# Optimization experiments

Hardware: AMD Instinct MI355X
Metric: run time of the kernel (lower is better)

Reference implementation:

```python
import jax, jax.numpy as jnp
import numpy as np

S = 512      # num_seg (queries)
T = 16384    # frames
D = 512      # d_model
DFF = 2048   # dim_feedforward
EPS = 1e-5


def layer_norm(x, g, b):
    mu = jnp.mean(x, axis=-1, keepdims=True)
    var = jnp.mean((x - mu) ** 2, axis=-1, keepdims=True)
    return (x - mu) * jax.lax.rsqrt(var + EPS) * g + b


def setup_inputs() -> dict:
    key = jax.random.key(0)
    ks = jax.random.split(key, 16)
    inv = 1.0 / np.sqrt(D)
    invf = 1.0 / np.sqrt(DFF)
    # action_idx: exactly S contiguous segments over T frames
    action_idx = (jnp.arange(T, dtype=jnp.int32) * S) // T
    return {
        "tgt": jax.random.normal(ks[0], (S, 1, D), jnp.float32),
        "memory": jax.random.normal(ks[1], (T, 1, D), jnp.float32),
        "pos": jax.random.normal(ks[2], (T, 1, D), jnp.float32),
        "query_pos": jax.random.normal(ks[3], (S, 1, D), jnp.float32),
        "action_idx": action_idx,
        "W_tgt2": jax.random.uniform(ks[4], (D, D), jnp.float32, -inv, inv),
        "b_tgt2": jax.random.uniform(ks[5], (D,), jnp.float32, -inv, inv),
        "W1": jax.random.uniform(ks[6], (DFF, D), jnp.float32, -inv, inv),
        "b1": jax.random.uniform(ks[7], (DFF,), jnp.float32, -inv, inv),
        "W2": jax.random.uniform(ks[8], (D, DFF), jnp.float32, -invf, invf),
        "b2": jax.random.uniform(ks[9], (D,), jnp.float32, -invf, invf),
        "g2": jnp.ones((D,), jnp.float32),
        "be2": jnp.zeros((D,), jnp.float32),
        "g3": jnp.ones((D,), jnp.float32),
        "be3": jnp.zeros((D,), jnp.float32),
    }


def reference(tgt, memory, pos, query_pos, action_idx,
              W_tgt2, b_tgt2, W1, b1, W2, b2, g2, be2, g3, be3):
    num_seg, _, dim = tgt.shape
    q = tgt + query_pos          # [S, 1, D]
    k = memory + pos             # [T, 1, D]
    v = memory                   # [T, 1, D]

    # segment-neighbor mask: seg_id per frame; query s attends to frames in
    # segments {s-1, s, s+1}
    change = jnp.concatenate([jnp.zeros((1,), jnp.int32),
                              (action_idx[1:] != action_idx[:-1]).astype(jnp.int32)])
    seg_id = jnp.cumsum(change)                                   # [T]
    mask = jnp.abs(seg_id[None, :] - jnp.arange(num_seg)[:, None]) <= 1  # [S, T]

    scores = jnp.einsum("sbd,tbd->bst", q, k) / np.sqrt(dim)      # [1, S, T]
    scores = jnp.where(mask[None], scores, -jnp.inf)
    attn = jax.nn.softmax(scores, axis=-1)                        # [1, S, T]

    ctx = jnp.einsum("bst,tbd->sbd", attn, v)                     # [S, 1, D]
    tgt2 = jax.nn.relu(ctx) @ W_tgt2.T + b_tgt2                   # [S, 1, D]
    x = layer_norm(tgt + tgt2, g2, be2)
    ffn = jax.nn.relu(x @ W1.T + b1) @ W2.T + b2
    out = layer_norm(x + ffn, g3, be3)
    return out
```

## Files before the change

### kernel.cpp

```cpp
#include <hip/hip_runtime.h>
#include <math.h>

#define S_Q  512
#define T_F  16384
#define D_M  512
#define DFF_ 2048
#define SEG  32
#define HSEG 16
#define SCALE 0.04419417382415922f

typedef __attribute__((ext_vector_type(8))) short short8;
typedef __attribute__((ext_vector_type(4))) float floatx4;

__device__ __forceinline__ unsigned short f2bf(float f) {
    unsigned int u = __builtin_bit_cast(unsigned int, f);
    u += 0x7FFFu + ((u >> 16) & 1u);
    return (unsigned short)(u >> 16);
}

__device__ __forceinline__ void async_copy16(const void* g, void* l) {
    __builtin_amdgcn_global_load_lds(
        (const __attribute__((address_space(1))) void*)g,
        (__attribute__((address_space(3))) void*)l, 16, 0, 0);
}

struct GSm { short A[2][2048]; short B[2][2048]; };

struct Params {
    const float *tgt, *memory, *pos, *qp;
    const float *b_tgt2, *b1, *b2, *g2, *be2, *g3, *be3;
    const float *W_tgt2, *W1, *W2;
    float *out;
    float *part; float2 *me;
    unsigned short *rc;
    float *gpart1, *x;
    unsigned short *xb, *h;
    float *gpart3;
    unsigned short *Wt2b, *W1b, *W2b;
};

__global__ __launch_bounds__(256, 4) void attn_conv(Params p)
{
    const int jb   = blockIdx.x;
    const int s    = jb >> 1;
    const int hh   = jb & 1;
    const int tid  = threadIdx.x;
    const int lane = tid & 63;
    const int wave = tid >> 6;

    __shared__ float v[HSEG * D_M];
    __shared__ float sc[3][HSEG];
    __shared__ float pr[3][HSEG];

    {
        const float* g = p.memory + (size_t)jb * HSEG * D_M
                       + (size_t)wave * 2048 + lane * 4;
        #pragma unroll
        for (int r = 0; r < 8; ++r)
            async_copy16(g + r * 256, v + wave * 2048 + r * 256);
    }

    float q0[8] = {}, q1[8] = {}, q2[8] = {};
    {
        const int d = lane * 8;
        if (s > 0) {
            const float4 a0 = *(const float4*)(p.tgt + (size_t)(s - 1) * D_M + d);
            const float4 a1 = *(const float4*)(p.tgt + (size_t)(s - 1) * D_M + d + 4);
            const float4 b0 = *(const float4*)(p.qp  + (size_t)(s - 1) * D_M + d);
            const float4 b1 = *(const float4*)(p.qp  + (size_t)(s - 1) * D_M + d + 4);
            q0[0]=a0.x+b0.x; q0[1]=a0.y+b0.y; q0[2]=a0.z+b0.z; q0[3]=a0.w+b0.w;
            q0[4]=a1.x+b1.x; q0[5]=a1.y+b1.y; q0[6]=a1.z+b1.z; q0[7]=a1.w+b1.w;
        }
        {
            const float4 a0 = *(const float4*)(p.tgt + (size_t)s * D_M + d);
            const float4 a1 = *(const float4*)(p.tgt + (size_t)s * D_M + d + 4);
            const float4 b0 = *(const float4*)(p.qp  + (size_t)s * D_M + d);
            const float4 b1 = *(const float4*)(p.qp  + (size_t)s * D_M + d + 4);
            q1[0]=a0.x+b0.x; q1[1]=a0.y+b0.y; q1[2]=a0.z+b0.z; q1[3]=a0.w+b0.w;
            q1[4]=a1.x+b1.x; q1[5]=a1.y+b1.y; q1[6]=a1.z+b1.z; q1[7]=a1.w+b1.w;
        }
        if (s < S_Q - 1) {
            const float4 a0 = *(const float4*)(p.tgt + (size_t)(s + 1) * D_M + d);
            const float4 a1 = *(const float4*)(p.tgt + (size_t)(s + 1) * D_M + d + 4);
            const float4 b0 = *(const float4*)(p.qp  + (size_t)(s + 1) * D_M + d);
            const float4 b1 = *(const float4*)(p.qp  + (size_t)(s + 1) * D_M + d + 4);
            q2[0]=a0.x+b0.x; q2[1]=a0.y+b0.y; q2[2]=a0.z+b0.z; q2[3]=a0.w+b0.w;
            q2[4]=a1.x+b1.x; q2[5]=a1.y+b1.y; q2[6]=a1.z+b1.z; q2[7]=a1.w+b1.w;
        }
    }
    __syncthreads();

    #pragma unroll
    for (int r = 0; r < 4; ++r) {
        const int f = wave * 4 + r;
        const size_t t = (size_t)(jb * HSEG + f);
        const float4 pA = *(const float4*)(p.pos + t * D_M + lane * 8);
        const float4 pB = *(const float4*)(p.pos + t * D_M + lane * 8 + 4);
        const float4 mA = *(const float4*)(v + f * D_M + lane * 8);
        const float4 mB = *(const float4*)(v + f * D_M + lane * 8 + 4);
        const float k8[8] = {mA.x+pA.x, mA.y+pA.y, mA.z+pA.z, mA.w+pA.w,
                             mB.x+pB.x, mB.y+pB.y, mB.z+pB.z, mB.w+pB.w};
        float a0 = 0.f, a1 = 0.f, a2 = 0.f;
        #pragma unroll
        for (int i = 0; i < 8; ++i) {
            a0 += k8[i] * q0[i]; a1 += k8[i] * q1[i]; a2 += k8[i] * q2[i];
        }
        #pragma unroll
        for (int off = 32; off > 0; off >>= 1) {
            a0 += __shfl_xor(a0, off, 64);
            a1 += __shfl_xor(a1, off, 64);
            a2 += __shfl_xor(a2, off, 64);
        }
        if (lane == 0) { sc[0][f] = a0 * SCALE; sc[1][f] = a1 * SCALE; sc[2][f] = a2 * SCALE; }
    }
    __syncthreads();

    if (wave < 3) {
        float mx = -1e30f;
        #pragma unroll
        for (int f = 0; f < HSEG; ++f) mx = fmaxf(mx, sc[wave][f]);
        float e = 0.f;
        #pragma unroll
        for (int f = 0; f < HSEG; ++f) {
            const float pe = __expf(sc[wave][f] - mx);
            e += pe;
            if (lane == 0) pr[wave][f] = pe;
        }
        const int q = s - 1 + wave;
        const int slot = hh + 4 - 2 * wave;
        if (lane == 0 && q >= 0 && q < S_Q)
            p.me[q * 6 + slot] = make_float2(mx, e);
    }
    __syncthreads();

    const int d0 = tid * 2;
    float c0x=0,c0y=0,c1x=0,c1y=0,c2x=0,c2y=0;
    #pragma unroll
    for (int f = 0; f < HSEG; ++f) {
        const float2 vv = *(const float2*)(v + f * D_M + d0);
        const float w0 = pr[0][f], w1 = pr[1][f], w2 = pr[2][f];
        c0x += w0 * vv.x; c0y += w0 * vv.y;
        c1x += w1 * vv.x; c1y += w1 * vv.y;
        c2x += w2 * vv.x; c2y += w2 * vv.y;
    }
    if (s > 0)
        *(float2*)(p.part + ((size_t)(s - 1) * 6 + 4 + hh) * D_M + d0) = make_float2(c0x, c0y);
    *(float2*)(p.part + ((size_t)s * 6 + 2 + hh) * D_M + d0) = make_float2(c1x, c1y);
    if (s < S_Q - 1)
        *(float2*)(p.part + ((size_t)(s + 1) * 6 + hh) * D_M + d0) = make_float2(c2x, c2y);

    {
        constexpr int n0 = D_M * D_M, n1 = DFF_ * D_M;
        constexpr int tot4 = (D_M * D_M + DFF_ * D_M + D_M * DFF_) / 4;
        for (int i4 = blockIdx.x * 256 + tid; i4 < tot4; i4 += 1024 * 256) {
            int i = i4 * 4;
            const float* src; unsigned short* dst;
            if (i < n0)            { src = p.W_tgt2; dst = p.Wt2b; }
            else if (i < n0 + n1)  { src = p.W1;     dst = p.W1b;  i -= n0; }
            else                   { src = p.W2;     dst = p.W2b;  i -= n0 + n1; }
            const float4 vv = *(const float4*)(src + i);
            unsigned short o[4] = {f2bf(vv.x), f2bf(vv.y), f2bf(vv.z), f2bf(vv.w)};
            *(uint2*)(dst + i) = *(const uint2*)o;
        }
    }
}

__global__ __launch_bounds__(256) void g_merge(Params p)
{
    const int row = blockIdx.x;
    const int tid = threadIdx.x;
    const int slo = (row == 0)       ? 2 : 0;
    const int shi = (row == S_Q - 1) ? 3 : 5;
    float mx = -1e30f;
    for (int s = slo; s <= shi; ++s) mx = fmaxf(mx, p.me[row * 6 + s].x);
    float den = 0.f, c[6] = {};
    for (int s = slo; s <= shi; ++s) {
        c[s] = __expf(p.me[row * 6 + s].x - mx);
        den += p.me[row * 6 + s].y * c[s];
    }
    const float inv = 1.f / den;
    const int d0 = tid * 2;
    float ax = 0.f, ay = 0.f;
    for (int s = slo; s <= shi; ++s) {
        const float2 pp = *(const float2*)(p.part + ((size_t)row * 6 + s) * D_M + d0);
        ax += c[s] * pp.x; ay += c[s] * pp.y;
    }
    const unsigned short o0 = f2bf(fmaxf(ax * inv, 0.f));
    const unsigned short o1 = f2bf(fmaxf(ay * inv, 0.f));
    *(unsigned int*)(p.rc + (size_t)row * D_M + d0) =
        (unsigned int)o0 | ((unsigned int)o1 << 16);
}

template<bool PARTIAL>
__device__ __forceinline__ void gemm_tile32(
    GSm* sg, const unsigned short* __restrict__ A, const unsigned short* __restrict__ B,
    int Nout, int K, int m0, int n0, int kbase, int niter,
    const float* __restrict__ bias, void* __restrict__ Cout, int zoff)
{
    const int tid  = threadIdx.x;
    const int lane = tid & 63;
    const int wave = tid >> 6;
    const int srow = tid >> 3;
    const int scol = (tid & 7) * 8;
    const int quad = lane >> 4;
    const int r16  = lane & 15;
    const int wm = (wave >> 1) * 16;
    const int wn = (wave & 1) * 16;

    floatx4 acc = {0.f, 0.f, 0.f, 0.f};

    async_copy16(A + (size_t)(m0 + srow) * K + kbase + scol, &sg->A[0][wave * 512]);
    async_copy16(B + (size_t)(n0 + srow) * K + kbase + scol, &sg->B[0][wave * 512]);

    for (int it = 0; it < niter; ++it) {
        __syncthreads();
        if (it + 1 < niter) {
            const int k0 = kbase + (it + 1) * 64;
            const int nb = (it + 1) & 1;
            async_copy16(A + (size_t)(m0 + srow) * K + k0 + scol, &sg->A[nb][wave * 512]);
            async_copy16(B + (size_t)(n0 + srow) * K + k0 + scol, &sg->B[nb][wave * 512]);
        }
        const short* Ab = sg->A[it & 1];
        const short* Bb = sg->B[it & 1];
        #pragma unroll
        for (int ks = 0; ks < 2; ++ks) {
            const short8 a = *(const short8*)(Ab + (wm + r16) * 64 + ks * 32 + quad * 8);
            const short8 b = *(const short8*)(Bb + (wn + r16) * 64 + ks * 32 + quad * 8);
            acc = __builtin_amdgcn_mfma_f32_16x16x32_bf16(a, b, acc, 0, 0, 0);
        }
    }

    const int col = n0 + wn + r16;
    const float bs = PARTIAL ? 0.f : bias[col];
    #pragma unroll
    for (int r = 0; r < 4; ++r) {
        const int row = m0 + wm + quad * 4 + r;
        float cv = acc[r];
        if (PARTIAL) {
            ((float*)Cout)[((size_t)(zoff + row)) * Nout + col] = cv;
        } else {
            cv = fmaxf(cv + bs, 0.f);
            ((unsigned short*)Cout)[(size_t)row * Nout + col] = f2bf(cv);
        }
    }
}

template<int NP, bool WRITE_BF16>
__device__ __forceinline__ void ln_rows(
    const float* __restrict__ parts, const float* __restrict__ res,
    const float* __restrict__ bias, const float* __restrict__ g,
    const float* __restrict__ be, float* __restrict__ out,
    unsigned short* __restrict__ out_bf, int rowblk)
{
    const int row  = rowblk * 4 + (threadIdx.x >> 6);
    const int lane = threadIdx.x & 63;

    float vv[8];
    #pragma unroll
    for (int hh = 0; hh < 2; ++hh) {
        const int d = lane * 8 + hh * 4;
        float4 a = *(const float4*)(res + (size_t)row * D_M + d);
        const float4 b = *(const float4*)(bias + d);
        a.x += b.x; a.y += b.y; a.z += b.z; a.w += b.w;
        #pragma unroll
        for (int z = 0; z < NP; ++z) {
            const float4 pp = *(const float4*)(parts + ((size_t)z * S_Q + row) * D_M + d);
            a.x += pp.x; a.y += pp.y; a.z += pp.z; a.w += pp.w;
        }
        vv[hh * 4 + 0] = a.x; vv[hh * 4 + 1] = a.y;
        vv[hh * 4 + 2] = a.z; vv[hh * 4 + 3] = a.w;
    }

    float sum = 0.f;
    #pragma unroll
    for (int i = 0; i < 8; ++i) sum += vv[i];
    #pragma unroll
    for (int off = 32; off > 0; off >>= 1) sum += __shfl_xor(sum, off, 64);
    const float mu = sum * (1.0f / 512.0f);

    float var = 0.f;
    #pragma unroll
    for (int i = 0; i < 8; ++i) { const float dd = vv[i] - mu; var += dd * dd; }
    #pragma unroll
    for (int off = 32; off > 0; off >>= 1) var += __shfl_xor(var, off, 64);
    const float rr = rsqrtf(var * (1.0f / 512.0f) + 1e-5f);

    #pragma unroll
    for (int hh = 0; hh < 2; ++hh) {
        const int d = lane * 8 + hh * 4;
        const float4 gg = *(const float4*)(g + d);
        const float4 bb = *(const float4*)(be + d);
        float4 o;
        o.x = (vv[hh*4+0] - mu) * rr * gg.x + bb.x;
        o.y = (vv[hh*4+1] - mu) * rr * gg.y + bb.y;
        o.z = (vv[hh*4+2] - mu) * rr * gg.z + bb.z;
        o.w = (vv[hh*4+3] - mu) * rr * gg.w + bb.w;
        *(float4*)(out + (size_t)row * D_M + d) = o;
        if (WRITE_BF16) {
            unsigned short ob[4] = {f2bf(o.x), f2bf(o.y), f2bf(o.z), f2bf(o.w)};
            *(uint2*)(out_bf + (size_t)row * D_M + d) = *(const uint2*)ob;
        }
    }
}

__global__ __launch_bounds__(256, 4) void g_gemm1(Params p) {
    __shared__ GSm sg;
    const int b = blockIdx.x;
    const int z = b >> 8, by = (b >> 4) & 15, bx = b & 15;
    gemm_tile32<true>(&sg, p.rc, p.Wt2b, D_M, D_M,
                      by * 32, bx * 32, z * 256, 4, nullptr, p.gpart1, z * S_Q);
}
__global__ __launch_bounds__(256) void g_ln1(Params p) {
    ln_rows<2, true>(p.gpart1, p.tgt, p.b_tgt2, p.g2, p.be2, p.x, p.xb, blockIdx.x);
}
__global__ __launch_bounds__(256, 4) void g_gemm2(Params p) {
    __shared__ GSm sg;
    const int t = blockIdx.x;
    gemm_tile32<false>(&sg, p.xb, p.W1b, DFF_, D_M,
                       (t >> 6) * 32, (t & 63) * 32, 0, 8, p.b1, p.h, 0);
}
__global__ __launch_bounds__(256, 4) void g_gemm3(Params p) {
    __shared__ GSm sg;
    const int b = blockIdx.x;
    const int z = b >> 8, by = (b >> 4) & 15, bx = b & 15;
    gemm_tile32<true>(&sg, p.h, p.W2b, D_M, DFF_,
                      by * 32, bx * 32, z * 512, 8, nullptr, p.gpart3, z * S_Q);
}
__global__ __launch_bounds__(256) void g_ln2(Params p) {
    ln_rows<4, false>(p.gpart3, p.x, p.b2, p.g3, p.be3, p.out, nullptr, blockIdx.x);
}

extern "C" void kernel_launch(void* const* d_in, const int* in_sizes, int n_in,
                              void* d_out, int out_size, void* d_ws, size_t ws_size,
                              hipStream_t stream) {
    Params p;
    p.tgt    = (const float*)d_in[0];
    p.memory = (const float*)d_in[1];
    p.pos    = (const float*)d_in[2];
    p.qp     = (const float*)d_in[3];
    p.W_tgt2 = (const float*)d_in[5];
    p.b_tgt2 = (const float*)d_in[6];
    p.W1     = (const float*)d_in[7];
    p.b1     = (const float*)d_in[8];
    p.W2     = (const float*)d_in[9];
    p.b2     = (const float*)d_in[10];
    p.g2     = (const float*)d_in[11];
    p.be2    = (const float*)d_in[12];
    p.g3     = (const float*)d_in[13];
    p.be3    = (const float*)d_in[14];
    p.out    = (float*)d_out;

    char* w = (char*)d_ws;
    size_t off = 0;
    p.part   = (float*)(w + off);          off += (size_t)S_Q * 6 * D_M * 4;
    p.me     = (float2*)(w + off);         off += (size_t)S_Q * 6 * 8;
    p.rc     = (unsigned short*)(w + off); off += (size_t)S_Q * D_M * 2;
    p.gpart1 = (float*)(w + off);          off += (size_t)2 * S_Q * D_M * 4;
    p.x      = (float*)(w + off);          off += (size_t)S_Q * D_M * 4;
    p.xb     = (unsigned short*)(w + off); off += (size_t)S_Q * D_M * 2;
    p.h      = (unsigned short*)(w + off); off += (size_t)S_Q * DFF_ * 2;
    p.gpart3 = (float*)(w + off);          off += (size_t)4 * S_Q * D_M * 4;
    p.Wt2b   = (unsigned short*)(w + off); off += (size_t)D_M * D_M * 2;
    p.W1b    = (unsigned short*)(w + off); off += (size_t)DFF_ * D_M * 2;
    p.W2b    = (unsigned short*)(w + off); off += (size_t)D_M * DFF_ * 2;

    attn_conv<<<1024, 256, 0, stream>>>(p);
    g_merge  <<<S_Q, 256, 0, stream>>>(p);
    g_gemm1  <<<512, 256, 0, stream>>>(p);
    g_ln1    <<<128, 256, 0, stream>>>(p);
    g_gemm2  <<<1024, 256, 0, stream>>>(p);
    g_gemm3  <<<1024, 256, 0, stream>>>(p);
    g_ln2    <<<128, 256, 0, stream>>>(p);
}
```

Baseline: 156.6 us.

## Split attention into quarter-segment blocks and drop max-rescaled softmax merge

```diff
diff --git a/kernel.cpp b/kernel.cpp
--- a/kernel.cpp
+++ b/kernel.cpp
@@ -6,7 +6,7 @@
 #define D_M  512
 #define DFF_ 2048
 #define SEG  32
-#define HSEG 16
+#define QSEG 8
 #define SCALE 0.04419417382415922f
 
 typedef __attribute__((ext_vector_type(8))) short short8;
@@ -31,7 +31,8 @@
     const float *b_tgt2, *b1, *b2, *g2, *be2, *g3, *be3;
     const float *W_tgt2, *W1, *W2;
     float *out;
-    float *part; float2 *me;
+    float *part;
+    float *den;
     unsigned short *rc;
     float *gpart1, *x;
     unsigned short *xb, *h;
@@ -39,25 +40,24 @@
     unsigned short *Wt2b, *W1b, *W2b;
 };
 
-__global__ __launch_bounds__(256, 4) void attn_conv(Params p)
+__global__ __launch_bounds__(256, 6) void attn_conv(Params p)
 {
     const int jb   = blockIdx.x;
-    const int s    = jb >> 1;
-    const int hh   = jb & 1;
+    const int s    = jb >> 2;
+    const int qh   = jb & 3;
     const int tid  = threadIdx.x;
     const int lane = tid & 63;
     const int wave = tid >> 6;
 
-    __shared__ float v[HSEG * D_M];
-    __shared__ float sc[3][HSEG];
-    __shared__ float pr[3][HSEG];
+    __shared__ float v[QSEG * D_M];
+    __shared__ float pr[3][QSEG];
 
     {
-        const float* g = p.memory + (size_t)jb * HSEG * D_M
-                       + (size_t)wave * 2048 + lane * 4;
-        #pragma unroll
-        for (int r = 0; r < 8; ++r)
-            async_copy16(g + r * 256, v + wave * 2048 + r * 256);
+        const float* g = p.memory + (size_t)jb * QSEG * D_M
+                       + (size_t)wave * 1024 + lane * 4;
+        #pragma unroll
+        for (int r = 0; r < 4; ++r)
+            async_copy16(g + r * 256, v + wave * 1024 + r * 256);
     }
 
     float q0[8] = {}, q1[8] = {}, q2[8] = {};
@@ -91,9 +91,9 @@
     __syncthreads();
 
     #pragma unroll
-    for (int r = 0; r < 4; ++r) {
-        const int f = wave * 4 + r;
-        const size_t t = (size_t)(jb * HSEG + f);
+    for (int r = 0; r < 2; ++r) {
+        const int f = wave * 2 + r;
+        const size_t t = (size_t)(jb * QSEG + f);
         const float4 pA = *(const float4*)(p.pos + t * D_M + lane * 8);
         const float4 pB = *(const float4*)(p.pos + t * D_M + lane * 8 + 4);
         const float4 mA = *(const float4*)(v + f * D_M + lane * 8);
@@ -111,32 +111,27 @@
             a1 += __shfl_xor(a1, off, 64);
             a2 += __shfl_xor(a2, off, 64);
         }
-        if (lane == 0) { sc[0][f] = a0 * SCALE; sc[1][f] = a1 * SCALE; sc[2][f] = a2 * SCALE; }
+        if (lane == 0) {
+            pr[0][f] = __expf(a0 * SCALE);
+            pr[1][f] = __expf(a1 * SCALE);
+            pr[2][f] = __expf(a2 * SCALE);
+        }
     }
     __syncthreads();
 
-    if (wave < 3) {
-        float mx = -1e30f;
-        #pragma unroll
-        for (int f = 0; f < HSEG; ++f) mx = fmaxf(mx, sc[wave][f]);
+    if (wave < 3 && lane == 0) {
         float e = 0.f;
         #pragma unroll
-        for (int f = 0; f < HSEG; ++f) {
-            const float pe = __expf(sc[wave][f] - mx);
-            e += pe;
-            if (lane == 0) pr[wave][f] = pe;
-        }
+        for (int f = 0; f < QSEG; ++f) e += pr[wave][f];
         const int q = s - 1 + wave;
-        const int slot = hh + 4 - 2 * wave;
-        if (lane == 0 && q >= 0 && q < S_Q)
-            p.me[q * 6 + slot] = make_float2(mx, e);
-    }
-    __syncthreads();
+        const int slot = qh + 4 * (2 - wave);
+        if (q >= 0 && q < S_Q) p.den[q * 12 + slot] = e;
+    }
 
     const int d0 = tid * 2;
     float c0x=0,c0y=0,c1x=0,c1y=0,c2x=0,c2y=0;
     #pragma unroll
-    for (int f = 0; f < HSEG; ++f) {
+    for (int f = 0; f < QSEG; ++f) {
         const float2 vv = *(const float2*)(v + f * D_M + d0);
         const float w0 = pr[0][f], w1 = pr[1][f], w2 = pr[2][f];
         c0x += w0 * vv.x; c0y += w0 * vv.y;
@@ -144,15 +139,15 @@
         c2x += w2 * vv.x; c2y += w2 * vv.y;
     }
     if (s > 0)
-        *(float2*)(p.part + ((size_t)(s - 1) * 6 + 4 + hh) * D_M + d0) = make_float2(c0x, c0y);
-    *(float2*)(p.part + ((size_t)s * 6 + 2 + hh) * D_M + d0) = make_float2(c1x, c1y);
+        *(float2*)(p.part + ((size_t)(s - 1) * 12 + 8 + qh) * D_M + d0) = make_float2(c0x, c0y);
+    *(float2*)(p.part + ((size_t)s * 12 + 4 + qh) * D_M + d0) = make_float2(c1x, c1y);
     if (s < S_Q - 1)
-        *(float2*)(p.part + ((size_t)(s + 1) * 6 + hh) * D_M + d0) = make_float2(c2x, c2y);
+        *(float2*)(p.part + ((size_t)(s + 1) * 12 + qh) * D_M + d0) = make_float2(c2x, c2y);
 
     {
         constexpr int n0 = D_M * D_M, n1 = DFF_ * D_M;
         constexpr int tot4 = (D_M * D_M + DFF_ * D_M + D_M * DFF_) / 4;
-        for (int i4 = blockIdx.x * 256 + tid; i4 < tot4; i4 += 1024 * 256) {
+        for (int i4 = blockIdx.x * 256 + tid; i4 < tot4; i4 += 2048 * 256) {
             int i = i4 * 4;
             const float* src; unsigned short* dst;
             if (i < n0)            { src = p.W_tgt2; dst = p.Wt2b; }
@@ -169,21 +164,18 @@
 {
     const int row = blockIdx.x;
     const int tid = threadIdx.x;
-    const int slo = (row == 0)       ? 2 : 0;
-    const int shi = (row == S_Q - 1) ? 3 : 5;
-    float mx = -1e30f;
-    for (int s = slo; s <= shi; ++s) mx = fmaxf(mx, p.me[row * 6 + s].x);
-    float den = 0.f, c[6] = {};
-    for (int s = slo; s <= shi; ++s) {
-        c[s] = __expf(p.me[row * 6 + s].x - mx);
-        den += p.me[row * 6 + s].y * c[s];
-    }
-    const float inv = 1.f / den;
+    const int slo = (row == 0)       ? 4 : 0;
+    const int shi = (row == S_Q - 1) ? 7 : 11;
+
+    float dsum = 0.f;
+    for (int s = slo; s <= shi; ++s) dsum += p.den[row * 12 + s];
+    const float inv = 1.f / dsum;
+
     const int d0 = tid * 2;
     float ax = 0.f, ay = 0.f;
     for (int s = slo; s <= shi; ++s) {
-        const float2 pp = *(const float2*)(p.part + ((size_t)row * 6 + s) * D_M + d0);
-        ax += c[s] * pp.x; ay += c[s] * pp.y;
+        const float2 pp = *(const float2*)(p.part + ((size_t)row * 12 + s) * D_M + d0);
+        ax += pp.x; ay += pp.y;
     }
     const unsigned short o0 = f2bf(fmaxf(ax * inv, 0.f));
     const unsigned short o1 = f2bf(fmaxf(ay * inv, 0.f));
@@ -352,8 +344,8 @@
 
     char* w = (char*)d_ws;
     size_t off = 0;
-    p.part   = (float*)(w + off);          off += (size_t)S_Q * 6 * D_M * 4;
-    p.me     = (float2*)(w + off);         off += (size_t)S_Q * 6 * 8;
+    p.part   = (float*)(w + off);          off += (size_t)S_Q * 12 * D_M * 4;
+    p.den    = (float*)(w + off);          off += (size_t)S_Q * 12 * 4;
     p.rc     = (unsigned short*)(w + off); off += (size_t)S_Q * D_M * 2;
     p.gpart1 = (float*)(w + off);          off += (size_t)2 * S_Q * D_M * 4;
     p.x      = (float*)(w + off);          off += (size_t)S_Q * D_M * 4;
@@ -364,7 +356,7 @@
     p.W1b    = (unsigned short*)(w + off); off += (size_t)DFF_ * D_M * 2;
     p.W2b    = (unsigned short*)(w + off); off += (size_t)D_M * DFF_ * 2;
 
-    attn_conv<<<1024, 256, 0, stream>>>(p);
+    attn_conv<<<2048, 256, 0, stream>>>(p);
     g_merge  <<<S_Q, 256, 0, stream>>>(p);
     g_gemm1  <<<512, 256, 0, stream>>>(p);
     g_ln1    <<<128, 256, 0, stream>>>(p);
```

Result: slower. 160.4 us (+2.4%).

## Drop softmax merge kernel via atomic unnormalized accumulation and deferred normalization

Applied to the files above, without the earlier changes.

```diff
diff --git a/kernel.cpp b/kernel.cpp
--- a/kernel.cpp
+++ b/kernel.cpp
@@ -24,15 +24,13 @@
         (__attribute__((address_space(3))) void*)l, 16, 0, 0);
 }
 
-struct GSm { short A[2][2048]; short B[2][2048]; };
-
 struct Params {
     const float *tgt, *memory, *pos, *qp;
     const float *b_tgt2, *b1, *b2, *g2, *be2, *g3, *be3;
     const float *W_tgt2, *W1, *W2;
     float *out;
-    float *part; float2 *me;
-    unsigned short *rc;
+    float *acc;
+    float *den;
     float *gpart1, *x;
     unsigned short *xb, *h;
     float *gpart3;
@@ -43,13 +41,11 @@
 {
     const int jb   = blockIdx.x;
     const int s    = jb >> 1;
-    const int hh   = jb & 1;
     const int tid  = threadIdx.x;
     const int lane = tid & 63;
     const int wave = tid >> 6;
 
     __shared__ float v[HSEG * D_M];
-    __shared__ float sc[3][HSEG];
     __shared__ float pr[3][HSEG];
 
     {
@@ -111,27 +107,21 @@
             a1 += __shfl_xor(a1, off, 64);
             a2 += __shfl_xor(a2, off, 64);
         }
-        if (lane == 0) { sc[0][f] = a0 * SCALE; sc[1][f] = a1 * SCALE; sc[2][f] = a2 * SCALE; }
+        if (lane == 0) {
+            pr[0][f] = __expf(a0 * SCALE);
+            pr[1][f] = __expf(a1 * SCALE);
+            pr[2][f] = __expf(a2 * SCALE);
+        }
     }
     __syncthreads();
 
-    if (wave < 3) {
-        float mx = -1e30f;
-        #pragma unroll
-        for (int f = 0; f < HSEG; ++f) mx = fmaxf(mx, sc[wave][f]);
+    if (wave < 3 && lane == 0) {
         float e = 0.f;
         #pragma unroll
-        for (int f = 0; f < HSEG; ++f) {
-            const float pe = __expf(sc[wave][f] - mx);
-            e += pe;
-            if (lane == 0) pr[wave][f] = pe;
-        }
+        for (int f = 0; f < HSEG; ++f) e += pr[wave][f];
         const int q = s - 1 + wave;
-        const int slot = hh + 4 - 2 * wave;
-        if (lane == 0 && q >= 0 && q < S_Q)
-            p.me[q * 6 + slot] = make_float2(mx, e);
-    }
-    __syncthreads();
+        if (q >= 0 && q < S_Q) atomicAdd(&p.den[q], e);
+    }
 
     const int d0 = tid * 2;
     float c0x=0,c0y=0,c1x=0,c1y=0,c2x=0,c2y=0;
@@ -143,11 +133,16 @@
         c1x += w1 * vv.x; c1y += w1 * vv.y;
         c2x += w2 * vv.x; c2y += w2 * vv.y;
     }
-    if (s > 0)
-        *(float2*)(p.part + ((size_t)(s - 1) * 6 + 4 + hh) * D_M + d0) = make_float2(c0x, c0y);
-    *(float2*)(p.part + ((size_t)s * 6 + 2 + hh) * D_M + d0) = make_float2(c1x, c1y);
-    if (s < S_Q - 1)
-        *(float2*)(p.part + ((size_t)(s + 1) * 6 + hh) * D_M + d0) = make_float2(c2x, c2y);
+    if (s > 0) {
+        atomicAdd(&p.acc[(size_t)(s - 1) * D_M + d0],     c0x);
+        atomicAdd(&p.acc[(size_t)(s - 1) * D_M + d0 + 1], c0y);
+    }
+    atomicAdd(&p.acc[(size_t)s * D_M + d0],     c1x);
+    atomicAdd(&p.acc[(size_t)s * D_M + d0 + 1], c1y);
+    if (s < S_Q - 1) {
+        atomicAdd(&p.acc[(size_t)(s + 1) * D_M + d0],     c2x);
+        atomicAdd(&p.acc[(size_t)(s + 1) * D_M + d0 + 1], c2y);
+    }
 
     {
         constexpr int n0 = D_M * D_M, n1 = DFF_ * D_M;
@@ -165,31 +160,73 @@
     }
 }
 
-__global__ __launch_bounds__(256) void g_merge(Params p)
+__global__ __launch_bounds__(256, 4) void g_gemm1(Params p)
 {
-    const int row = blockIdx.x;
-    const int tid = threadIdx.x;
-    const int slo = (row == 0)       ? 2 : 0;
-    const int shi = (row == S_Q - 1) ? 3 : 5;
-    float mx = -1e30f;
-    for (int s = slo; s <= shi; ++s) mx = fmaxf(mx, p.me[row * 6 + s].x);
-    float den = 0.f, c[6] = {};
-    for (int s = slo; s <= shi; ++s) {
-        c[s] = __expf(p.me[row * 6 + s].x - mx);
-        den += p.me[row * 6 + s].y * c[s];
-    }
-    const float inv = 1.f / den;
-    const int d0 = tid * 2;
-    float ax = 0.f, ay = 0.f;
-    for (int s = slo; s <= shi; ++s) {
-        const float2 pp = *(const float2*)(p.part + ((size_t)row * 6 + s) * D_M + d0);
-        ax += c[s] * pp.x; ay += c[s] * pp.y;
-    }
-    const unsigned short o0 = f2bf(fmaxf(ax * inv, 0.f));
-    const unsigned short o1 = f2bf(fmaxf(ay * inv, 0.f));
-    *(unsigned int*)(p.rc + (size_t)row * D_M + d0) =
-        (unsigned int)o0 | ((unsigned int)o1 << 16);
-}
+    __shared__ float Af[2][32 * 64];
+    __shared__ short Bs[2][32 * 64];
+
+    const int b = blockIdx.x;
+    const int z = b >> 8, by = (b >> 4) & 15, bx = b & 15;
+    const int m0 = by * 32, n0 = bx * 32, kbase = z * 256;
+    const int tid  = threadIdx.x;
+    const int lane = tid & 63;
+    const int wave = tid >> 6;
+    const int quad = lane >> 4;
+    const int r16  = lane & 15;
+    const int wm = (wave >> 1) * 16;
+    const int wn = (wave & 1) * 16;
+
+    const int arow = (lane >> 4);
+    const int acol = (lane & 15) * 4;
+    const int brow = tid >> 3;
+    const int bcol = (tid & 7) * 8;
+
+    floatx4 acc4 = {0.f, 0.f, 0.f, 0.f};
+
+    auto stageA = [&](int buf, int k0) {
+        #pragma unroll
+        for (int c = 0; c < 2; ++c) {
+            const int row = wave * 8 + c * 4 + arow;
+            async_copy16(p.acc + (size_t)(m0 + row) * D_M + k0 + acol,
+                         &Af[buf][(wave * 8 + c * 4) * 64]);
+        }
+    };
+    auto stageB = [&](int buf, int k0) {
+        async_copy16(p.Wt2b + (size_t)(n0 + brow) * D_M + k0 + bcol,
+                     &Bs[buf][wave * 512]);
+    };
+
+    stageA(0, kbase); stageB(0, kbase);
+
+    for (int it = 0; it < 4; ++it) {
+        __syncthreads();
+        if (it + 1 < 4) { stageA((it + 1) & 1, kbase + (it + 1) * 64);
+                          stageB((it + 1) & 1, kbase + (it + 1) * 64); }
+        const float* Ab = Af[it & 1];
+        const short* Bb = Bs[it & 1];
+        #pragma unroll
+        for (int ks = 0; ks < 2; ++ks) {
+            const float4 fa0 = *(const float4*)(Ab + (wm + r16) * 64 + ks * 32 + quad * 8);
+            const float4 fa1 = *(const float4*)(Ab + (wm + r16) * 64 + ks * 32 + quad * 8 + 4);
+            short8 a;
+            a[0] = (short)f2bf(fmaxf(fa0.x, 0.f)); a[1] = (short)f2bf(fmaxf(fa0.y, 0.f));
+            a[2] = (short)f2bf(fmaxf(fa0.z, 0.f)); a[3] = (short)f2bf(fmaxf(fa0.w, 0.f));
+            a[4] = (short)f2bf(fmaxf(fa1.x, 0.f)); a[5] = (short)f2bf(fmaxf(fa1.y, 0.f));
+            a[6] = (short)f2bf(fmaxf(fa1.z, 0.f)); a[7] = (short)f2bf(fmaxf(fa1.w, 0.f));
+            const short8 bb = *(const short8*)(Bb + (wn + r16) * 64 + ks * 32 + quad * 8);
+            acc4 = __builtin_amdgcn_mfma_f32_16x16x32_bf16(a, bb, acc4, 0, 0, 0);
+        }
+    }
+
+    const int col = n0 + wn + r16;
+    #pragma unroll
+    for (int r = 0; r < 4; ++r) {
+        const int row = m0 + wm + quad * 4 + r;
+        p.gpart1[((size_t)(z * S_Q + row)) * D_M + col] = acc4[r];
+    }
+}
+
+struct GSm { short A[2][2048]; short B[2][2048]; };
 
 template<bool PARTIAL>
 __device__ __forceinline__ void gemm_tile32(
@@ -245,15 +282,16 @@
     }
 }
 
-template<int NP, bool WRITE_BF16>
+template<int NP, bool WRITE_BF16, bool DEN_SCALE>
 __device__ __forceinline__ void ln_rows(
-    const float* __restrict__ parts, const float* __restrict__ res,
-    const float* __restrict__ bias, const float* __restrict__ g,
-    const float* __restrict__ be, float* __restrict__ out,
-    unsigned short* __restrict__ out_bf, int rowblk)
+    const float* __restrict__ parts, const float* __restrict__ den,
+    const float* __restrict__ res, const float* __restrict__ bias,
+    const float* __restrict__ g, const float* __restrict__ be,
+    float* __restrict__ out, unsigned short* __restrict__ out_bf, int rowblk)
 {
     const int row  = rowblk * 4 + (threadIdx.x >> 6);
     const int lane = threadIdx.x & 63;
+    const float sc = DEN_SCALE ? (1.0f / den[row]) : 1.0f;
 
     float vv[8];
     #pragma unroll
@@ -262,11 +300,13 @@
         float4 a = *(const float4*)(res + (size_t)row * D_M + d);
         const float4 b = *(const float4*)(bias + d);
         a.x += b.x; a.y += b.y; a.z += b.z; a.w += b.w;
+        float4 ps = {0.f, 0.f, 0.f, 0.f};
         #pragma unroll
         for (int z = 0; z < NP; ++z) {
             const float4 pp = *(const float4*)(parts + ((size_t)z * S_Q + row) * D_M + d);
-            a.x += pp.x; a.y += pp.y; a.z += pp.z; a.w += pp.w;
-        }
+            ps.x += pp.x; ps.y += pp.y; ps.z += pp.z; ps.w += pp.w;
+        }
+        a.x += sc * ps.x; a.y += sc * ps.y; a.z += sc * ps.z; a.w += sc * ps.w;
         vv[hh * 4 + 0] = a.x; vv[hh * 4 + 1] = a.y;
         vv[hh * 4 + 2] = a.z; vv[hh * 4 + 3] = a.w;
     }
@@ -303,15 +343,9 @@
     }
 }
 
-__global__ __launch_bounds__(256, 4) void g_gemm1(Params p) {
-    __shared__ GSm sg;
-    const int b = blockIdx.x;
-    const int z = b >> 8, by = (b >> 4) & 15, bx = b & 15;
-    gemm_tile32<true>(&sg, p.rc, p.Wt2b, D_M, D_M,
-                      by * 32, bx * 32, z * 256, 4, nullptr, p.gpart1, z * S_Q);
-}
 __global__ __launch_bounds__(256) void g_ln1(Params p) {
-    ln_rows<2, true>(p.gpart1, p.tgt, p.b_tgt2, p.g2, p.be2, p.x, p.xb, blockIdx.x);
+    ln_rows<2, true, true>(p.gpart1, p.den, p.tgt, p.b_tgt2,
+                           p.g2, p.be2, p.x, p.xb, blockIdx.x);
 }
 __global__ __launch_bounds__(256, 4) void g_gemm2(Params p) {
     __shared__ GSm sg;
@@ -327,7 +361,8 @@
                       by * 32, bx * 32, z * 512, 8, nullptr, p.gpart3, z * S_Q);
 }
 __global__ __launch_bounds__(256) void g_ln2(Params p) {
-    ln_rows<4, false>(p.gpart3, p.x, p.b2, p.g3, p.be3, p.out, nullptr, blockIdx.x);
+    ln_rows<4, false, false>(p.gpart3, nullptr, p.x, p.b2,
+                             p.g3, p.be3, p.out, nullptr, blockIdx.x);
 }
 
 extern "C" void kernel_launch(void* const* d_in, const int* in_sizes, int n_in,
@@ -352,9 +387,8 @@
 
     char* w = (char*)d_ws;
     size_t off = 0;
-    p.part   = (float*)(w + off);          off += (size_t)S_Q * 6 * D_M * 4;
-    p.me     = (float2*)(w + off);         off += (size_t)S_Q * 6 * 8;
-    p.rc     = (unsigned short*)(w + off); off += (size_t)S_Q * D_M * 2;
+    p.acc    = (float*)(w + off);          off += (size_t)S_Q * D_M * 4;
+    p.den    = (float*)(w + off);          off += (size_t)S_Q * 4;
     p.gpart1 = (float*)(w + off);          off += (size_t)2 * S_Q * D_M * 4;
     p.x      = (float*)(w + off);          off += (size_t)S_Q * D_M * 4;
     p.xb     = (unsigned short*)(w + off); off += (size_t)S_Q * D_M * 2;
@@ -364,8 +398,9 @@
     p.W1b    = (unsigned short*)(w + off); off += (size_t)DFF_ * D_M * 2;
     p.W2b    = (unsigned short*)(w + off); off += (size_t)D_M * DFF_ * 2;
 
+    hipMemsetAsync(p.acc, 0, (size_t)(S_Q * D_M + S_Q) * 4, stream);
+
     attn_conv<<<1024, 256, 0, stream>>>(p);
-    g_merge  <<<S_Q, 256, 0, stream>>>(p);
     g_gemm1  <<<512, 256, 0, stream>>>(p);
     g_ln1    <<<128, 256, 0, stream>>>(p);
     g_gemm2  <<<1024, 256, 0, stream>>>(p);
```

New measurement: 162.6 us. 1.04x slower.
